# Optimization experiments

Hardware: AMD Instinct MI355X
Metric: run time of the kernel (lower is better)

The kernel has to match this reference:

```python
import jax, jax.numpy as jnp
import numpy as np

DIM = 1024
Q_HEADS = 16
KV_HEADS = 4
DIM_HEAD = DIM // Q_HEADS  # 64
SOFTCLAMP = 50.0
EPS = 1e-8


def rotate_half(x):
    x_even = x[..., ::2]
    x_odd = x[..., 1::2]
    return jnp.stack([-x_odd, x_even], axis=-1).reshape(x.shape)


def setup_inputs() -> dict:
    key = jax.random.key(0)
    ks = jax.random.split(key, 10)
    B, S = 1, 2048
    dim_q = DIM_HEAD * Q_HEADS   # 1024
    dim_kv = DIM_HEAD * KV_HEADS  # 256
    std = 0.02
    x = jax.random.normal(ks[0], (B, S, DIM), dtype=jnp.float32)
    positions = jnp.broadcast_to(jnp.arange(S, dtype=jnp.int32)[None, :], (B, S))
    # causal mask: True = disallowed (torch semantics: allowed = ~attn_mask)
    attn_mask = jnp.triu(jnp.ones((S, S), dtype=bool), k=1)
    return {
        "x": x,
        "positions": positions,
        "attn_mask": attn_mask,
        "Wq": jax.random.normal(ks[1], (DIM, dim_q), jnp.float32) * std,
        "Wk": jax.random.normal(ks[2], (DIM, dim_kv), jnp.float32) * std,
        "Wv": jax.random.normal(ks[3], (DIM, dim_kv), jnp.float32) * std,
        "Wo": jax.random.normal(ks[4], (dim_q, DIM), jnp.float32) * std,
        "Wg": jax.random.normal(ks[5], (DIM, Q_HEADS), jnp.float32) * std,
        "Wm": jax.random.normal(ks[6], (DIM, KV_HEADS), jnp.float32) * std,
        "bm": jnp.zeros((KV_HEADS,), jnp.float32),
        "Wvr": jax.random.normal(ks[7], (DIM, dim_kv), jnp.float32) * std,
        "k_scale": jnp.ones((KV_HEADS, DIM_HEAD), jnp.float32),
    }


def reference(x, positions, attn_mask, Wq, Wk, Wv, Wo, Wg, Wm, bm, Wvr, k_scale):
    b, s, _ = x.shape
    h, qh, dh = KV_HEADS, Q_HEADS, DIM_HEAD
    g = qh // h

    q = (x @ Wq).reshape(b, s, qh, dh).transpose(0, 2, 1, 3)  # [b,qh,s,dh]
    k = (x @ Wk).reshape(b, s, h, dh).transpose(0, 2, 1, 3)   # [b,h,s,dh]
    v = (x @ Wv).reshape(b, s, h, dh).transpose(0, 2, 1, 3)

    # value-residual gating: v = lerp(v, residual_v, mix)
    residual_v = (x @ Wvr).reshape(b, s, h, dh).transpose(0, 2, 1, 3)
    mix = jax.nn.sigmoid(x @ Wm + bm).transpose(0, 2, 1)[..., None]  # [b,h,s,1]
    v = v + mix * (residual_v - v)

    # multi-head RMSNorm on k
    rms = jnp.sqrt(jnp.mean(k * k, axis=-1, keepdims=True) + EPS)
    k = k / rms * k_scale[None, :, None, :]

    # rotary embeddings (identical for all heads -> broadcast over head dim)
    inv_freq = 1.0 / (10000.0 ** (jnp.arange(0, dh, 2, dtype=jnp.float32) / dh))
    freqs = positions.astype(jnp.float32)[..., None] * inv_freq  # [b,s,dh/2]
    cos = jnp.repeat(jnp.cos(freqs), 2, axis=-1)[:, None, :, :]  # [b,1,s,dh]
    sin = jnp.repeat(jnp.sin(freqs), 2, axis=-1)[:, None, :, :]
    q = q * cos + rotate_half(q) * sin
    k = k * cos + rotate_half(k) * sin

    # grouped-query attention with softclamped scores
    scale = dh ** -0.5
    qg = q.reshape(b, h, g, s, dh)
    sim = jnp.einsum('bhgqd,bhkd->bhgqk', qg, k) * scale
    sim = jnp.tanh(sim / SOFTCLAMP) * SOFTCLAMP
    allowed = ~attn_mask  # [s,s]
    sim = jnp.where(allowed[None, None, None, :, :], sim, jnp.finfo(sim.dtype).min)
    attn = jax.nn.softmax(sim, axis=-1)
    out = jnp.einsum('bhgqk,bhkd->bhgqd', attn, v).reshape(b, qh, s, dh)

    # per-query-head sigmoid gates
    gates = jax.nn.sigmoid(x @ Wg).transpose(0, 2, 1)[..., None]  # [b,qh,s,1]
    out = out * gates

    out = out.transpose(0, 2, 1, 3).reshape(b, s, qh * dh)
    return out @ Wo
```

## Files before the change

kernel.cpp:

```cpp
#include <hip/hip_runtime.h>
#include <hip/hip_bf16.h>
#include <math.h>

typedef unsigned short u16;
typedef unsigned int u32;
typedef __attribute__((ext_vector_type(8))) __bf16 bf16x8;
typedef __attribute__((ext_vector_type(4))) float f32x4;

__device__ inline u16 f2bf(float f) {
  u32 b = __float_as_uint(f);
  b += 0x7FFFu + ((b >> 16) & 1u);
  return (u16)(b >> 16);
}
__device__ inline float bf2f(u16 b) { return __uint_as_float((u32)b << 16); }

__device__ __forceinline__ void gll16(const void* gp, void* lp) {
  __builtin_amdgcn_global_load_lds(
      (const __attribute__((address_space(1))) void*)gp,
      (__attribute__((address_space(3))) void*)lp, 16, 0, 0);
}

__global__ __launch_bounds__(256) void prep_all_k(
    const float* __restrict__ x, const int* __restrict__ positions,
    const float* __restrict__ Wq, const float* __restrict__ Wk,
    const float* __restrict__ Wv, const float* __restrict__ Wvr,
    const float* __restrict__ Wo, const float* __restrict__ Wg,
    const float* __restrict__ Wm, u16* __restrict__ xb,
    u16* __restrict__ WallT, u16* __restrict__ WoT, float* __restrict__ rtab) {
  __shared__ float tile[32][33];
  int bid = blockIdx.x, tid = threadIdx.x;
  if (bid < 1024) {
    int i = (bid * 256 + tid) * 8;
    float4 v0 = *(const float4*)&x[i];
    float4 v1 = *(const float4*)&x[i + 4];
    uint4 pk;
    pk.x = (u32)f2bf(v0.x) | ((u32)f2bf(v0.y) << 16);
    pk.y = (u32)f2bf(v0.z) | ((u32)f2bf(v0.w) << 16);
    pk.z = (u32)f2bf(v1.x) | ((u32)f2bf(v1.y) << 16);
    pk.w = (u32)f2bf(v1.z) | ((u32)f2bf(v1.w) << 16);
    *(uint4*)&xb[i] = pk;
    return;
  }
  if (bid >= 3968) {
    int idx = (bid - 3968) * 256 + tid;
    int s = idx >> 5, f = idx & 31;
    float inv = __expf(-(float)f * (9.210340371976184f / 32.f));
    float ang = (float)positions[s] * inv;
    rtab[(size_t)s * 64 + f] = cosf(ang);
    rtab[(size_t)s * 64 + 32 + f] = sinf(ang);
    return;
  }
  int b2 = bid - 1024;
  int k0 = (b2 & 31) * 32;
  int ybl = b2 >> 5;
  int tx = tid & 31, ty = tid >> 5;
  const float* src;
  int scol, sN, drow;
  u16* dst;
  if (ybl >= 60) {
    src = Wo; scol = (ybl - 60) * 32; sN = 1024; dst = WoT; drow = scol;
  } else {
    int n0 = ybl * 32;
    if (n0 >= 1792) {
#pragma unroll
      for (int j = 0; j < 4; ++j) {
        int n = n0 + ty * 4 + j, j2 = n - 1792, k = k0 + tx;
        float val = (j2 < 16) ? Wg[(size_t)k * 16 + j2]
                  : (j2 < 20) ? Wm[(size_t)k * 4 + (j2 - 16)] : 0.f;
        WallT[(size_t)n * 1024 + k] = f2bf(val);
      }
      return;
    }
    dst = WallT; drow = n0;
    if (n0 < 1024) { src = Wq; scol = n0; sN = 1024; }
    else if (n0 < 1280) { src = Wk; scol = n0 - 1024; sN = 256; }
    else if (n0 < 1536) { src = Wv; scol = n0 - 1280; sN = 256; }
    else { src = Wvr; scol = n0 - 1536; sN = 256; }
  }
#pragma unroll
  for (int j = 0; j < 4; ++j)
    tile[ty * 4 + j][tx] = src[(size_t)(k0 + ty * 4 + j) * sN + scol + tx];
  __syncthreads();
#pragma unroll
  for (int j = 0; j < 4; ++j)
    dst[(size_t)(drow + ty * 4 + j) * 1024 + k0 + tx] = f2bf(tile[tx][ty * 4 + j]);
}

template <int BM, bool BF16_OUT>
__global__ __launch_bounds__(512) void gemm_bf16_k(
    const u16* __restrict__ A, const u16* __restrict__ Bt, void* __restrict__ Cv,
    int M, int N, int K) {
  constexpr int MI = BM / 32;
  __shared__ __align__(16) u16 As[2][BM * 64];
  __shared__ __align__(16) u16 Bs[2][128 * 64];
  int tid = threadIdx.x;
  int w = tid >> 6, l = tid & 63;
  int wr = w >> 2, wc = w & 3;
  int lr = l & 15, lg = l >> 4;
  int lrow = l >> 3, lcol = (l & 7) * 8;
  int m0 = blockIdx.y * BM, n0 = blockIdx.x * 128;
  f32x4 zero = {0.f, 0.f, 0.f, 0.f};
  f32x4 acc[MI][2];
#pragma unroll
  for (int mi = 0; mi < MI; ++mi)
#pragma unroll
    for (int ni = 0; ni < 2; ++ni) acc[mi][ni] = zero;

  auto gstage = [&](int buf, int kt) {
#pragma unroll
    for (int ts = 0; ts < BM / 64; ++ts) {
      int seg = ts * 8 + w;
      gll16(&A[(size_t)(m0 + seg * 8 + lrow) * K + kt + lcol],
            &As[buf][seg * 512]);
    }
#pragma unroll
    for (int ts = 0; ts < 2; ++ts) {
      int seg = ts * 8 + w;
      gll16(&Bt[(size_t)(n0 + seg * 8 + lrow) * K + kt + lcol],
            &Bs[buf][seg * 512]);
    }
  };

  gstage(0, 0);
  __syncthreads();
  int nt = K >> 6;
#pragma unroll 1
  for (int t = 0; t < nt; ++t) {
    int cur = t & 1;
    if (t + 1 < nt) gstage(cur ^ 1, (t + 1) * 64);
#pragma unroll
    for (int kw = 0; kw < 2; ++kw) {
      bf16x8 af[MI], bfr[2];
#pragma unroll
      for (int mi = 0; mi < MI; ++mi)
        af[mi] = *(const bf16x8*)&As[cur][(wr * (BM / 2) + mi * 16 + lr) * 64 + kw * 32 + lg * 8];
#pragma unroll
      for (int ni = 0; ni < 2; ++ni)
        bfr[ni] = *(const bf16x8*)&Bs[cur][(wc * 32 + ni * 16 + lr) * 64 + kw * 32 + lg * 8];
#pragma unroll
      for (int mi = 0; mi < MI; ++mi)
#pragma unroll
        for (int ni = 0; ni < 2; ++ni)
          acc[mi][ni] = __builtin_amdgcn_mfma_f32_16x16x32_bf16(
              af[mi], bfr[ni], acc[mi][ni], 0, 0, 0);
    }
    __syncthreads();
  }
#pragma unroll
  for (int mi = 0; mi < MI; ++mi)
#pragma unroll
    for (int ni = 0; ni < 2; ++ni)
#pragma unroll
      for (int r = 0; r < 4; ++r) {
        int row = m0 + wr * (BM / 2) + mi * 16 + lg * 4 + r;
        int col = n0 + wc * 32 + ni * 16 + lr;
        if (BF16_OUT)
          ((u16*)Cv)[(size_t)row * N + col] = f2bf(acc[mi][ni][r]);
        else
          ((float*)Cv)[(size_t)row * N + col] = acc[mi][ni][r];
      }
}

__global__ __launch_bounds__(256) void postproc_k(
    const float* __restrict__ bm, const float* __restrict__ ksc,
    const float* __restrict__ rtab, u16* __restrict__ qkvrb,
    u16* __restrict__ kb, u16* __restrict__ vb, float* __restrict__ g_out) {
  int s = blockIdx.x, tid = threadIdx.x;
  int lane = tid & 63, w = tid >> 6;
  u16* row = qkvrb + (size_t)s * 1920;
  const float* tr = rtab + (size_t)s * 64;
  if (tid < 16)
    g_out[s * 16 + tid] = 1.f / (1.f + __expf(-bf2f(row[1792 + tid])));
  int h = w, d = lane;
  float c = tr[d >> 1], sn = tr[32 + (d >> 1)];
  {
    float mixv = 1.f / (1.f + __expf(-(bf2f(row[1808 + h]) + bm[h])));
    float vv = bf2f(row[1280 + h * 64 + d]);
    float rv = bf2f(row[1536 + h * 64 + d]);
    vb[((size_t)h * 2048 + s) * 64 + d] = f2bf(vv + mixv * (rv - vv));
  }
  {
    float kv = bf2f(row[1024 + h * 64 + d]);
    float ss = kv * kv;
#pragma unroll
    for (int off = 32; off > 0; off >>= 1) ss += __shfl_xor(ss, off);
    float rms = sqrtf(ss * (1.f / 64.f) + 1e-8f);
    float kn = kv / rms * ksc[h * 64 + d];
    float partner = __shfl_xor(kn, 1);
    kb[((size_t)h * 2048 + s) * 64 + d] =
        f2bf((d & 1) ? fmaf(kn, c, partner * sn) : fmaf(kn, c, -partner * sn));
  }
#pragma unroll
  for (int r = 0; r < 4; ++r) {
    int e = r * 256 + tid;
    int dq = e & 63;
    float cq = tr[dq >> 1], sq = tr[32 + (dq >> 1)];
    float qv = bf2f(row[e]);
    float partner = __shfl_xor(qv, 1);
    float qr = (e & 1) ? fmaf(qv, cq, partner * sq) : fmaf(qv, cq, -partner * sq);
    row[e] = f2bf(qr * 0.125f);
  }
}

#define TPAD 66
__global__ __launch_bounds__(256) void vtrans_k(const u16* __restrict__ vb,
                                               u16* __restrict__ vtb) {
  __shared__ u16 tile[64 * TPAD];
  int h = blockIdx.y, s0 = blockIdx.x * 64;
  int t = threadIdx.x;
  {
    int r = t >> 2, cb = (t & 3) * 16;
    const u16* src = vb + ((size_t)h * 2048 + s0 + r) * 64 + cb;
    *(uint4*)&tile[r * TPAD + cb] = *(const uint4*)src;
    *(uint4*)&tile[r * TPAD + cb + 8] = *(const uint4*)(src + 8);
  }
  __syncthreads();
  int d = t >> 2, sb = (t & 3) * 16;
  u16 vals[16];
#pragma unroll
  for (int j = 0; j < 16; ++j) vals[j] = tile[(sb + j) * TPAD + d];
  uint4 a, b;
  a.x = (u32)vals[0] | ((u32)vals[1] << 16);
  a.y = (u32)vals[2] | ((u32)vals[3] << 16);
  a.z = (u32)vals[4] | ((u32)vals[5] << 16);
  a.w = (u32)vals[6] | ((u32)vals[7] << 16);
  b.x = (u32)vals[8] | ((u32)vals[9] << 16);
  b.y = (u32)vals[10] | ((u32)vals[11] << 16);
  b.z = (u32)vals[12] | ((u32)vals[13] << 16);
  b.w = (u32)vals[14] | ((u32)vals[15] << 16);
  u16* dst = vtb + ((size_t)h * 64 + d) * 2048 + s0 + sb;
  *(uint4*)dst = a;
  *(uint4*)(dst + 8) = b;
}

__global__ __launch_bounds__(512) void attn_k(
    const u16* __restrict__ qkvrb, const u16* __restrict__ kb,
    const u16* __restrict__ vtb, const float* __restrict__ g,
    u16* __restrict__ aob) {
  __shared__ __align__(16) u16 smem[40960];
  int head = blockIdx.x, hkv = head >> 2;
  int tid = threadIdx.x;
  int w = tid >> 6, l = tid & 63;
  int grp = w >> 2, wi = w & 3;
  int lr = l & 15, lg = l >> 4;
  int gtid = wi * 64 + l;
  u16* KsBase = smem + grp * 16384;
  u32* pw = (u32*)(smem + 32768) + (size_t)w * 512;
  float* mbuf = (float*)smem;
  f32x4 zero = {0.f, 0.f, 0.f, 0.f};
  const float L2E = 1.4426950408889634f;
  const float NB = -72.13475204444817f;
  int sw = (lr & 7) << 2;
  int u0 = ((lg ^ (lr & 7)) << 3);
  int srow = l >> 3;
  int sunit = (l & 7) ^ srow;
  const u16* ksrc = kb + ((size_t)hkv * 2048 + srow) * 64 + sunit * 8;
  const u16* vsrc = vtb + ((size_t)(hkv * 64 + srow)) * 2048 + sunit * 8;
#pragma unroll 1
  for (int half = 0; half < 2; ++half) {
    int rb = half ? (int)blockIdx.y : (31 - (int)blockIdx.y);
    int row0 = rb * 64;
    const u16* qrow = qkvrb + (size_t)(row0 + wi * 16 + lr) * 1920 + head * 64;
    bf16x8 qf0 = *(const bf16x8*)&qrow[lg * 8];
    bf16x8 qf1 = *(const bf16x8*)&qrow[32 + lg * 8];
    f32x4 acc_o[4];
#pragma unroll
    for (int nd = 0; nd < 4; ++nd) acc_o[nd] = zero;
    float l_part = 0.f;
    int qglob = row0 + wi * 16 + lr;
    int c = grp;
    if (c <= rb) {
#pragma unroll
      for (int t = 0; t < 2; ++t) {
        int seg = wi * 2 + t;
        gll16(ksrc + (size_t)(c * 64 + seg * 8) * 64, KsBase + seg * 512);
        gll16(vsrc + (size_t)(seg * 8) * 2048 + c * 64,
              KsBase + 4096 + seg * 512);
      }
    }
    __syncthreads();
    int nmax = (rb >> 1) + 1;
#pragma unroll 1
    for (int i = 0; i < nmax; ++i, c += 2) {
      bool valid = (c <= rb);
      if (c + 2 <= rb) {
        u16* Ksn = KsBase + ((i & 1) ^ 1) * 8192;
        int nc = c + 2;
#pragma unroll
        for (int t = 0; t < 2; ++t) {
          int seg = wi * 2 + t;
          gll16(ksrc + (size_t)(nc * 64 + seg * 8) * 64, Ksn + seg * 512);
          gll16(vsrc + (size_t)(seg * 8) * 2048 + nc * 64,
                Ksn + 4096 + seg * 512);
        }
      }
      if (valid) {
        u16* Ks = KsBase + (i & 1) * 8192;
        u16* Vt = Ks + 4096;
        int kbase = c * 64;
        __builtin_amdgcn_s_setprio(1);
        f32x4 sa[4];
#pragma unroll
        for (int ni = 0; ni < 4; ++ni) {
          const u16* kp = &Ks[(ni * 16 + lr) * 64];
          bf16x8 a0 = *(const bf16x8*)&kp[u0];
          bf16x8 a1 = *(const bf16x8*)&kp[u0 ^ 32];
          f32x4 t = __builtin_amdgcn_mfma_f32_16x16x32_bf16(a0, qf0, zero, 0, 0, 0);
          sa[ni] = __builtin_amdgcn_mfma_f32_16x16x32_bf16(a1, qf1, t, 0, 0, 0);
        }
        bool diag = (c == rb);
#pragma unroll
        for (int ni = 0; ni < 4; ++ni) {
          float pv[4];
#pragma unroll
          for (int r = 0; r < 4; ++r) {
            float sv = fminf(fmaxf(sa[ni][r], -60.f), 60.f);
            float t2 = sv * 0.02f;
            float u = t2 * t2;
            float cl = sv * fmaf(u, fmaf(u, 0.13333333f, -0.33333333f), 1.f);
            float p = __builtin_amdgcn_exp2f(fmaf(cl, L2E, NB));
            if (diag && (kbase + ni * 16 + lg * 4 + r) > qglob) p = 0.f;
            pv[r] = p;
            l_part += p;
          }
          u32 w0, w1;
          asm("v_cvt_pk_bf16_f32 %0, %1, %2" : "=v"(w0) : "v"(pv[0]), "v"(pv[1]));
          asm("v_cvt_pk_bf16_f32 %0, %1, %2" : "=v"(w1) : "v"(pv[2]), "v"(pv[3]));
          uint2 pr;
          pr.x = w0;
          pr.y = w1;
          *(uint2*)&pw[lr * 32 + ((ni * 8 + lg * 2) ^ sw)] = pr;
        }
        bf16x8 pfa = *(const bf16x8*)&pw[lr * 32 + ((lg * 4) ^ sw)];
        bf16x8 pfb = *(const bf16x8*)&pw[lr * 32 + ((16 + lg * 4) ^ sw)];
#pragma unroll
        for (int nd = 0; nd < 4; ++nd) {
          const u16* vp = &Vt[(nd * 16 + lr) * 64];
          bf16x8 v0 = *(const bf16x8*)&vp[u0];
          bf16x8 v1 = *(const bf16x8*)&vp[u0 ^ 32];
          acc_o[nd] = __builtin_amdgcn_mfma_f32_16x16x32_bf16(pfa, v0, acc_o[nd], 0, 0, 0);
          acc_o[nd] = __builtin_amdgcn_mfma_f32_16x16x32_bf16(pfb, v1, acc_o[nd], 0, 0, 0);
        }
        __builtin_amdgcn_s_setprio(0);
      }
      __syncthreads();
    }
    l_part += __shfl_xor(l_part, 16);
    l_part += __shfl_xor(l_part, 32);
    if (grp == 1) {
      float* mb = mbuf + (size_t)gtid * 17;
#pragma unroll
      for (int nd = 0; nd < 4; ++nd)
#pragma unroll
        for (int r = 0; r < 4; ++r) mb[nd * 4 + r] = acc_o[nd][r];
      mb[16] = l_part;
    }
    __syncthreads();
    if (grp == 0) {
      const float* mb = mbuf + (size_t)gtid * 17;
      float lt = l_part + mb[16];
#pragma unroll
      for (int r = 0; r < 4; ++r) {
        int row = row0 + wi * 16 + lg * 4 + r;
        float lv = __shfl(lt, lg * 4 + r);
        float sc = g[row * 16 + head] * __builtin_amdgcn_rcpf(lv);
#pragma unroll
        for (int nd = 0; nd < 4; ++nd)
          aob[(size_t)row * 1024 + head * 64 + nd * 16 + lr] =
              f2bf((acc_o[nd][r] + mb[nd * 4 + r]) * sc);
      }
    }
    __syncthreads();
  }
}

extern "C" void kernel_launch(void* const* d_in, const int* in_sizes, int n_in,
                              void* d_out, int out_size, void* d_ws,
                              size_t ws_size, hipStream_t stream) {
  const float* x = (const float*)d_in[0];
  const int* positions = (const int*)d_in[1];
  const float* Wq = (const float*)d_in[3];
  const float* Wk = (const float*)d_in[4];
  const float* Wv = (const float*)d_in[5];
  const float* Wo = (const float*)d_in[6];
  const float* Wg = (const float*)d_in[7];
  const float* Wm = (const float*)d_in[8];
  const float* bm = (const float*)d_in[9];
  const float* Wvr = (const float*)d_in[10];
  const float* ksc = (const float*)d_in[11];
  float* out = (float*)d_out;

  u16* xb = (u16*)d_ws;
  u16* WallT = xb + (size_t)2048 * 1024;
  u16* WoT = WallT + (size_t)1920 * 1024;
  u16* qkvrb = WoT + (size_t)1024 * 1024;
  u16* kbuf = qkvrb + (size_t)2048 * 1920;
  u16* vbuf = kbuf + (size_t)4 * 2048 * 64;
  u16* vtb = vbuf + (size_t)4 * 2048 * 64;
  float* gbuf = (float*)(vtb + (size_t)4 * 2048 * 64);
  float* rtab = gbuf + (size_t)2048 * 16;
  u16* aob = xb;

  prep_all_k<<<4224, 256, 0, stream>>>(x, positions, Wq, Wk, Wv, Wvr, Wo, Wg,
                                       Wm, xb, WallT, WoT, rtab);
  gemm_bf16_k<128, true><<<dim3(15, 16), 512, 0, stream>>>(xb, WallT, qkvrb,
                                                           2048, 1920, 1024);
  postproc_k<<<2048, 256, 0, stream>>>(bm, ksc, rtab, qkvrb, kbuf, vbuf, gbuf);
  vtrans_k<<<dim3(32, 4), 256, 0, stream>>>(vbuf, vtb);
  attn_k<<<dim3(16, 16), 512, 0, stream>>>(qkvrb, kbuf, vtb, gbuf, aob);
  gemm_bf16_k<64, false><<<dim3(8, 32), 512, 0, stream>>>(aob, WoT, out, 2048,
                                                          1024, 1024);
}
```

Measured before the change: 88.71 us.

## Triple-buffer K/V staging in attention with partial vmcnt waits

Moves the K/V LDS staging in the attention kernel from double to triple buffering, prefetching two chunks ahead. The blanket __syncthreads is replaced by s_waitcnt vmcnt(4) plus s_barrier, so one chunk's loads can stay in flight across the barrier. The aim is to hide global-load latency better. In exchange LDS use rises from 80KB to 112KB per block, and correctness depends on the hand-counted vmcnt matching the number of outstanding loads.

```diff
diff --git a/kernel.cpp b/kernel.cpp
--- a/kernel.cpp
+++ b/kernel.cpp
@@ -237,15 +237,15 @@
     const u16* __restrict__ qkvrb, const u16* __restrict__ kb,
     const u16* __restrict__ vtb, const float* __restrict__ g,
     u16* __restrict__ aob) {
-  __shared__ __align__(16) u16 smem[40960];
+  __shared__ __align__(16) u16 smem[57344];
   int head = blockIdx.x, hkv = head >> 2;
   int tid = threadIdx.x;
   int w = tid >> 6, l = tid & 63;
   int grp = w >> 2, wi = w & 3;
   int lr = l & 15, lg = l >> 4;
   int gtid = wi * 64 + l;
-  u16* KsBase = smem + grp * 16384;
-  u32* pw = (u32*)(smem + 32768) + (size_t)w * 512;
+  u16* KsBase = smem + grp * 24576;
+  u32* pw = (u32*)(smem + 49152) + (size_t)w * 512;
   float* mbuf = (float*)smem;
   f32x4 zero = {0.f, 0.f, 0.f, 0.f};
   const float L2E = 1.4426950408889634f;
@@ -256,6 +256,15 @@
   int sunit = (l & 7) ^ srow;
   const u16* ksrc = kb + ((size_t)hkv * 2048 + srow) * 64 + sunit * 8;
   const u16* vsrc = vtb + ((size_t)(hkv * 64 + srow)) * 2048 + sunit * 8;
+  auto stageChunk = [&](int b, int cc) {
+    u16* Kb = KsBase + b * 8192;
+#pragma unroll
+    for (int t = 0; t < 2; ++t) {
+      int seg = wi * 2 + t;
+      gll16(ksrc + (size_t)(cc * 64 + seg * 8) * 64, Kb + seg * 512);
+      gll16(vsrc + (size_t)(seg * 8) * 2048 + cc * 64, Kb + 4096 + seg * 512);
+    }
+  };
 #pragma unroll 1
   for (int half = 0; half < 2; ++half) {
     int rb = half ? (int)blockIdx.y : (31 - (int)blockIdx.y);
@@ -269,33 +278,26 @@
     float l_part = 0.f;
     int qglob = row0 + wi * 16 + lr;
     int c = grp;
-    if (c <= rb) {
-#pragma unroll
-      for (int t = 0; t < 2; ++t) {
-        int seg = wi * 2 + t;
-        gll16(ksrc + (size_t)(c * 64 + seg * 8) * 64, KsBase + seg * 512);
-        gll16(vsrc + (size_t)(seg * 8) * 2048 + c * 64,
-              KsBase + 4096 + seg * 512);
-      }
-    }
-    __syncthreads();
+    if (c <= rb) stageChunk(0, c);
+    if (c + 2 <= rb) {
+      stageChunk(1, c + 2);
+      asm volatile("s_waitcnt vmcnt(4)\n\ts_barrier" ::: "memory");
+    } else {
+      asm volatile("s_waitcnt vmcnt(0)\n\ts_barrier" ::: "memory");
+    }
     int nmax = (rb >> 1) + 1;
+    int bufc = 0;
 #pragma unroll 1
     for (int i = 0; i < nmax; ++i, c += 2) {
       bool valid = (c <= rb);
-      if (c + 2 <= rb) {
-        u16* Ksn = KsBase + ((i & 1) ^ 1) * 8192;
-        int nc = c + 2;
-#pragma unroll
-        for (int t = 0; t < 2; ++t) {
-          int seg = wi * 2 + t;
-          gll16(ksrc + (size_t)(nc * 64 + seg * 8) * 64, Ksn + seg * 512);
-          gll16(vsrc + (size_t)(seg * 8) * 2048 + nc * 64,
-                Ksn + 4096 + seg * 512);
-        }
+      bool sn = (c + 4 <= rb);
+      if (sn) {
+        int bufs = bufc - 1;
+        if (bufs < 0) bufs = 2;
+        stageChunk(bufs, c + 4);
       }
       if (valid) {
-        u16* Ks = KsBase + (i & 1) * 8192;
+        u16* Ks = KsBase + bufc * 8192;
         u16* Vt = Ks + 4096;
         int kbase = c * 64;
         __builtin_amdgcn_s_setprio(1);
@@ -343,7 +345,12 @@
         }
         __builtin_amdgcn_s_setprio(0);
       }
-      __syncthreads();
+      if (sn) {
+        asm volatile("s_waitcnt vmcnt(4)\n\ts_barrier" ::: "memory");
+      } else {
+        asm volatile("s_waitcnt vmcnt(0)\n\ts_barrier" ::: "memory");
+      }
+      bufc = (bufc == 2) ? 0 : bufc + 1;
     }
     l_part += __shfl_xor(l_part, 16);
     l_part += __shfl_xor(l_part, 32);
```

Result: no change. 88.43 us (-0.3%).
